# Kernel tuning notes

Hardware: AMD Instinct MI355X
Metric: run time of the kernel (lower is better)

## Reference

```python
import jax, jax.numpy as jnp
import numpy as np

B, S, D_IN, D_H, D_OUT = 32, 1024, 512, 512, 512
N_HEADS, K_NEI = 2, 3
LN_EPS = 1e-5


def _layernorm(x, g, b):
    mu = x.mean(-1, keepdims=True)
    xc = x - mu
    var = (xc * xc).mean(-1, keepdims=True)
    return xc * jax.lax.rsqrt(var + LN_EPS) * g + b


def setup_inputs() -> dict:
    key = jax.random.key(0)
    ks = jax.random.split(key, 8)
    sc = 0.02
    rn = lambda k, shape: jax.random.normal(k, shape, jnp.float32) * sc
    return {
        "x": jax.random.normal(ks[0], (B, S, D_IN), jnp.float32),
        "enc_w": rn(ks[1], (D_H, D_IN)), "enc_b": jnp.zeros((D_H,), jnp.float32),
        "in_w": rn(ks[2], (3 * D_H, D_H)), "in_b": jnp.zeros((3 * D_H,), jnp.float32),
        "out_w": rn(ks[3], (D_H, D_H)), "out_b": jnp.zeros((D_H,), jnp.float32),
        "ln1_g": jnp.ones((D_H,), jnp.float32), "ln1_b": jnp.zeros((D_H,), jnp.float32),
        "ffn_w1": rn(ks[4], (2 * D_H, D_H)), "ffn_b1": jnp.zeros((2 * D_H,), jnp.float32),
        "ffn_w2": rn(ks[5], (D_H, 2 * D_H)), "ffn_b2": jnp.zeros((D_H,), jnp.float32),
        "gc_w": rn(ks[6], (D_H, 2 * D_H)), "gc_b": jnp.zeros((D_H,), jnp.float32),
        "ln2_g": jnp.ones((D_H,), jnp.float32), "ln2_b": jnp.zeros((D_H,), jnp.float32),
        "dec_w": rn(ks[7], (D_OUT, D_H)), "dec_b": jnp.zeros((D_OUT,), jnp.float32),
    }


def reference(x, enc_w, enc_b, in_w, in_b, out_w, out_b, ln1_g, ln1_b,
              ffn_w1, ffn_b1, ffn_w2, ffn_b2, gc_w, gc_b, ln2_g, ln2_b,
              dec_w, dec_b):
    # --- encoder ---
    h = jax.nn.relu(x @ enc_w.T + enc_b)                          # [B,S,Dh]

    # --- ElevateH0toH1: self-attention + LN + residual FFN ---
    qkv = h @ in_w.T + in_b                                       # [B,S,3Dh]
    q, k, v = jnp.split(qkv, 3, axis=-1)
    dh = D_H // N_HEADS
    heads = lambda t: t.reshape(B, S, N_HEADS, dh).transpose(0, 2, 1, 3)
    q, k, v = heads(q), heads(k), heads(v)
    scores = jnp.einsum("bhqd,bhkd->bhqk", q, k) / jnp.sqrt(jnp.float32(dh))
    attn = jax.nn.softmax(scores, axis=-1)
    ctx = jnp.einsum("bhqk,bhkd->bhqd", attn, v)
    ctx = ctx.transpose(0, 2, 1, 3).reshape(B, S, D_H)
    attn_out = ctx @ out_w.T + out_b
    x1 = _layernorm(h + attn_out, ln1_g, ln1_b)
    x1 = x1 + (jax.nn.relu(x1 @ ffn_w1.T + ffn_b1) @ ffn_w2.T + ffn_b2)

    # --- ElevateH1toH2: symmetric KNN adjacency from cosine similarity ---
    nrm = x1 / jnp.maximum(jnp.linalg.norm(x1, axis=-1, keepdims=True), 1e-12)
    sim = jnp.einsum("bid,bjd->bij", nrm, nrm)                    # [B,S,S]
    kk = min(K_NEI, S - 1)
    _, idx = jax.lax.top_k(sim, kk + 1)                           # [B,S,k+1] (incl. self)
    mask = jnp.zeros((B, S, S), bool).at[
        jnp.arange(B)[:, None, None], jnp.arange(S)[None, :, None], idx
    ].set(True)
    mask = mask & ~jnp.eye(S, dtype=bool)                         # drop self edges
    mask = mask | mask.transpose(0, 2, 1)                         # symmetrize
    adj = jnp.where(mask, sim, jnp.float32(0.0))

    nsum = jnp.einsum("bij,bjd->bid", adj, x1)
    cnt = jnp.maximum(adj.sum(-1, keepdims=True), jnp.float32(1.0))
    combined = jnp.concatenate([x1, nsum / cnt], axis=-1)         # [B,S,2Dh]
    out = combined @ gc_w.T + gc_b
    x2 = _layernorm(x1 + out, ln2_g, ln2_b)

    # --- pool + decoder ---
    return x2.mean(axis=1) @ dec_w.T + dec_b                      # [B,D_OUT]
```

## Files before the change

### kernel.cpp

```cpp
#include <hip/hip_runtime.h>
#include <hip/hip_bf16.h>
#include <math.h>

typedef unsigned short u16;
typedef __attribute__((ext_vector_type(8))) short bfrag;
typedef __attribute__((ext_vector_type(4))) float facc;
typedef const __attribute__((address_space(1))) void* gaddr_t;
typedef __attribute__((address_space(3))) void* laddr_t;

#define F_RELU   1
#define F_ROWSC  4
#define F_SIMSC  8
#define F_RESID2 32

__device__ __forceinline__ u16 f2bf(float f) {
  __hip_bfloat16 h = __float2bfloat16(f);
  return *reinterpret_cast<u16*>(&h);
}
__device__ __forceinline__ float bf2f(u16 u) {
  __hip_bfloat16 h = *reinterpret_cast<__hip_bfloat16*>(&u);
  return __bfloat162float(h);
}
__device__ __forceinline__ float wsum(float v) {
#pragma unroll
  for (int o = 32; o; o >>= 1) v += __shfl_xor(v, o);
  return v;
}
__device__ __forceinline__ float wmaxf(float v) {
#pragma unroll
  for (int o = 32; o; o >>= 1) v = fmaxf(v, __shfl_xor(v, o));
  return v;
}

struct GSeg {
  const u16* A; const u16* B;
  long sA, sB;
  int lda, ldb, K;
  int hA, hB;
};

__global__ __launch_bounds__(256)
void bgemm_k(GSeg s0, GSeg s1, GSeg s2, int nseg,
             const float* __restrict__ bias,
             const u16* __restrict__ residH, const u16* __restrict__ residL,
             const float* __restrict__ rsc, const float* __restrict__ csc,
             float* __restrict__ Cf, u16* __restrict__ Cb, u16* __restrict__ Cb2,
             int ldc, long sC, int hC, int headBits, int sS,
             float alpha, int flags, int Mstore)
{
  const int zAll = blockIdx.z;
  const int hIdx = headBits ? (zAll & 1) : 0;
  const int z    = headBits ? (zAll >> 1) : zAll;
  const long cofs = (long)z * sC + (long)hIdx * hC;
  const float* rs = rsc ? rsc + (long)z * sS : nullptr;
  const float* cs = csc ? csc + (long)z * sS : nullptr;

  __shared__ u16 As[128 * 64];
  __shared__ u16 Bs[128 * 64];

  const int tid  = threadIdx.x;
  const int wave = tid >> 6, lane = tid & 63;
  const int m0 = blockIdx.x * 128, n0 = blockIdx.y * 128;
  const int wrow = (wave >> 1) * 64, wcol = (wave & 1) * 64;

  const int lrow = lane >> 3;
  const int lgrp = lane & 7;

  facc acc[4][4];
#pragma unroll
  for (int i = 0; i < 4; ++i)
#pragma unroll
    for (int j = 0; j < 4; ++j) acc[i][j] = (facc)(0.f);

  const int r16 = lane & 15, gq = lane >> 4;

  for (int seg = 0; seg < nseg; ++seg) {
    const GSeg& S = seg == 0 ? s0 : (seg == 1 ? s1 : s2);
    const u16* Ab = S.A + (long)z * S.sA + (long)hIdx * S.hA;
    const u16* Bb = S.B + (long)z * S.sB + (long)hIdx * S.hB;
    for (int k0 = 0; k0 < S.K; k0 += 64) {
#pragma unroll
      for (int ss = 0; ss < 4; ++ss) {
        int rloc = wave * 32 + ss * 8;
        int row  = rloc + lrow;
        int g    = lgrp ^ ((row >> 1) & 7);
        __builtin_amdgcn_global_load_lds(
            (gaddr_t)(const void*)(Ab + (long)(m0 + row) * S.lda + k0 + g * 8),
            (laddr_t)(As + rloc * 64), 16, 0, 0);
        __builtin_amdgcn_global_load_lds(
            (gaddr_t)(const void*)(Bb + (long)(n0 + row) * S.ldb + k0 + g * 8),
            (laddr_t)(Bs + rloc * 64), 16, 0, 0);
      }
      __syncthreads();

#pragma unroll
      for (int kk = 0; kk < 2; ++kk) {
        bfrag af[4], bb[4];
#pragma unroll
        for (int mt = 0; mt < 4; ++mt) {
          int r = wrow + mt * 16 + r16;
          int slot = (kk * 4 + gq) ^ ((r >> 1) & 7);
          af[mt] = *(const bfrag*)&As[r * 64 + slot * 8];
        }
#pragma unroll
        for (int nt = 0; nt < 4; ++nt) {
          int r = wcol + nt * 16 + r16;
          int slot = (kk * 4 + gq) ^ ((r >> 1) & 7);
          bb[nt] = *(const bfrag*)&Bs[r * 64 + slot * 8];
        }
#pragma unroll
        for (int mt = 0; mt < 4; ++mt)
#pragma unroll
          for (int nt = 0; nt < 4; ++nt)
            acc[mt][nt] = __builtin_amdgcn_mfma_f32_16x16x32_bf16(
                af[mt], bb[nt], acc[mt][nt], 0, 0, 0);
      }
      __syncthreads();
    }
  }

#pragma unroll
  for (int mt = 0; mt < 4; ++mt) {
#pragma unroll
    for (int nt = 0; nt < 4; ++nt) {
#pragma unroll
      for (int r = 0; r < 4; ++r) {
        int gm = m0 + wrow + mt * 16 + gq * 4 + r;
        int gn = n0 + wcol + nt * 16 + r16;
        if (gm >= Mstore) continue;
        float v = acc[mt][nt][r] * alpha;
        long ci = cofs + (long)gm * ldc + gn;
        if (flags & F_SIMSC)  v *= rs[gm] * cs[gn];
        if (flags & F_ROWSC)  v *= rs[gm];
        if (bias)             v += bias[gn];
        if (flags & F_RESID2) v += bf2f(residH[ci]) + bf2f(residL[ci]);
        if (flags & F_RELU)   v = fmaxf(v, 0.f);
        if (Cf) Cf[ci] = v;
        if (Cb) {
          u16 hv = f2bf(v);
          Cb[ci] = hv;
          if (Cb2) Cb2[ci] = f2bf(v - bf2f(hv));
        }
      }
    }
  }
}

__global__ __launch_bounds__(256)
void castbf_k(const float* __restrict__ in, u16* __restrict__ out, int n)
{
  int i = blockIdx.x * 256 + threadIdx.x;
  if (i < n) out[i] = f2bf(in[i]);
}

__global__ __launch_bounds__(256)
void castw_k(const float* w0, const float* w1, const float* w2,
             const float* w3, const float* w4, const float* w5,
             const float* w6, u16* __restrict__ dst)
{
  int i = blockIdx.x * 256 + threadIdx.x;
  const float* s; int off;
  if      (i < 262144)  { s = w0; off = 0; }
  else if (i < 1048576) { s = w1; off = 262144; }
  else if (i < 1310720) { s = w2; off = 1048576; }
  else if (i < 1835008) { s = w3; off = 1310720; }
  else if (i < 2359296) { s = w4; off = 1835008; }
  else if (i < 2883584) { s = w5; off = 2359296; }
  else                  { s = w6; off = 2883584; }
  dst[i] = f2bf(s[i - off]);
}

__global__ __launch_bounds__(256)
void ln1_k(const u16* __restrict__ a, const u16* __restrict__ b,
           const float* __restrict__ g, const float* __restrict__ be,
           u16* __restrict__ oh, u16* __restrict__ ol)
{
  long base = (long)blockIdx.x * 512;
  int t = threadIdx.x;
  float v0 = bf2f(a[base + t])       + bf2f(b[base + t]);
  float v1 = bf2f(a[base + t + 256]) + bf2f(b[base + t + 256]);
  __shared__ float red[4], red2[4];
  float s = wsum(v0 + v1);
  if ((t & 63) == 0) red[t >> 6] = s;
  __syncthreads();
  float mean = (red[0] + red[1] + red[2] + red[3]) * (1.f / 512.f);
  float c0 = v0 - mean, c1 = v1 - mean;
  float ss = wsum(c0 * c0 + c1 * c1);
  if ((t & 63) == 0) red2[t >> 6] = ss;
  __syncthreads();
  float var = (red2[0] + red2[1] + red2[2] + red2[3]) * (1.f / 512.f);
  float rstd = rsqrtf(var + 1e-5f);
  float o0 = c0 * rstd * g[t]       + be[t];
  float o1 = c1 * rstd * g[t + 256] + be[t + 256];
  u16 h0 = f2bf(o0), h1 = f2bf(o1);
  oh[base + t] = h0;       oh[base + t + 256] = h1;
  ol[base + t] = f2bf(o0 - bf2f(h0));
  ol[base + t + 256] = f2bf(o1 - bf2f(h1));
}

__global__ __launch_bounds__(256)
void ln2_k(const u16* __restrict__ hi, const u16* __restrict__ lo,
           const u16* __restrict__ b, const float* __restrict__ g,
           const float* __restrict__ be, u16* __restrict__ ob)
{
  long base = (long)blockIdx.x * 512;
  int t = threadIdx.x;
  float v0 = bf2f(hi[base + t])       + bf2f(lo[base + t])       + bf2f(b[base + t]);
  float v1 = bf2f(hi[base + t + 256]) + bf2f(lo[base + t + 256]) + bf2f(b[base + t + 256]);
  __shared__ float red[4], red2[4];
  float s = wsum(v0 + v1);
  if ((t & 63) == 0) red[t >> 6] = s;
  __syncthreads();
  float mean = (red[0] + red[1] + red[2] + red[3]) * (1.f / 512.f);
  float c0 = v0 - mean, c1 = v1 - mean;
  float ss = wsum(c0 * c0 + c1 * c1);
  if ((t & 63) == 0) red2[t >> 6] = ss;
  __syncthreads();
  float var = (red2[0] + red2[1] + red2[2] + red2[3]) * (1.f / 512.f);
  float rstd = rsqrtf(var + 1e-5f);
  ob[base + t]       = f2bf(c0 * rstd * g[t]       + be[t]);
  ob[base + t + 256] = f2bf(c1 * rstd * g[t + 256] + be[t + 256]);
}

__global__ __launch_bounds__(256)
void rownorm_k(const u16* __restrict__ hi, const u16* __restrict__ lo,
               float* __restrict__ invn)
{
  long base = (long)blockIdx.x * 512;
  int t = threadIdx.x;
  float v0 = bf2f(hi[base + t])       + bf2f(lo[base + t]);
  float v1 = bf2f(hi[base + t + 256]) + bf2f(lo[base + t + 256]);
  __shared__ float red[4];
  float s = wsum(v0 * v0 + v1 * v1);
  if ((t & 63) == 0) red[t >> 6] = s;
  __syncthreads();
  if (t == 0) {
    float tot = red[0] + red[1] + red[2] + red[3];
    invn[blockIdx.x] = 1.f / fmaxf(sqrtf(tot), 1e-12f);
  }
}

__global__ __launch_bounds__(256)
void softmaxu_k(u16* __restrict__ sc)
{
  long row = blockIdx.x;
  u16* p = sc + row * 1024;
  int t = threadIdx.x;
  float v[4];
#pragma unroll
  for (int i = 0; i < 4; ++i) v[i] = bf2f(p[t + 256 * i]);
  __shared__ float redm[4], redsum[4];
  float m4 = fmaxf(fmaxf(v[0], v[1]), fmaxf(v[2], v[3]));
  float wm = wmaxf(m4);
  if ((t & 63) == 0) redm[t >> 6] = wm;
  __syncthreads();
  float MX = fmaxf(fmaxf(redm[0], redm[1]), fmaxf(redm[2], redm[3]));
  float s = 0.f;
#pragma unroll
  for (int i = 0; i < 4; ++i) { v[i] = __expf(v[i] - MX); s += v[i]; }
  float ws_ = wsum(s);
  if ((t & 63) == 0) redsum[t >> 6] = ws_;
  __syncthreads();
  float inv = 1.f / (redsum[0] + redsum[1] + redsum[2] + redsum[3]);
#pragma unroll
  for (int i = 0; i < 4; ++i) p[t + 256 * i] = f2bf(v[i] * inv);
}

__global__ __launch_bounds__(256)
void transp_k(const u16* __restrict__ in, u16* __restrict__ out,
              int inStride, int outStride, long sIn, long sOut,
              int hIn, int headBits)
{
  const int zAll = blockIdx.z;
  const int h  = headBits ? (zAll & 1) : 0;
  const int zb = headBits ? (zAll >> 1) : zAll;
  const u16* src = in + (long)zb * sIn + (long)h * hIn;
  u16* dst = out + (long)zAll * sOut;
  const int r0 = blockIdx.x * 64, c0 = blockIdx.y * 64;
  __shared__ u16 tile[64][66];
  const int t = threadIdx.x;
#pragma unroll
  for (int p = 0; p < 16; ++p) {
    int idx = p * 256 + t;
    int r = idx >> 6, c = idx & 63;
    tile[r][c] = src[(long)(r0 + r) * inStride + c0 + c];
  }
  __syncthreads();
#pragma unroll
  for (int p = 0; p < 16; ++p) {
    int idx = p * 256 + t;
    int c = idx >> 6, r = idx & 63;
    dst[(long)(c0 + c) * outStride + r0 + r] = tile[r][c];
  }
}

__global__ __launch_bounds__(64)
void topk_k(const float* __restrict__ sim, int* __restrict__ idx4)
{
  long row = blockIdx.x;
  const float* p = sim + row * 1024;
  int t = threadIdx.x;
  int c0 = -1, c1 = -1, c2 = -1, c3 = -1;
#pragma unroll
  for (int pass = 0; pass < 4; ++pass) {
    float best = -INFINITY;
    int bi = 1 << 30;
    for (int j = t; j < 1024; j += 64) {
      if (j == c0 || j == c1 || j == c2 || j == c3) continue;
      float v = p[j];
      if (v > best || (v == best && j < bi)) { best = v; bi = j; }
    }
#pragma unroll
    for (int off = 32; off; off >>= 1) {
      float ov = __shfl_down(best, off);
      int   oi = __shfl_down(bi, off);
      if (ov > best || (ov == best && oi < bi)) { best = ov; bi = oi; }
    }
    bi = __shfl(bi, 0);
    if (pass == 0) c0 = bi; else if (pass == 1) c1 = bi;
    else if (pass == 2) c2 = bi; else c3 = bi;
  }
  if (t == 0) { int* q = idx4 + row * 4; q[0] = c0; q[1] = c1; q[2] = c2; q[3] = c3; }
}

__global__ __launch_bounds__(256)
void adjbf_k(const float* __restrict__ sim, const int* __restrict__ idx4,
             u16* __restrict__ adjb, float* __restrict__ invcnt)
{
  long row = blockIdx.x;
  int b = (int)(row >> 10);
  int i = (int)(row & 1023);
  const float* prow = sim + row * 1024;
  u16* arow_ = adjb + row * 1024;
  const int* my = idx4 + row * 4;
  int m0 = my[0], m1 = my[1], m2 = my[2], m3 = my[3];
  int t = threadIdx.x;
  float lsum = 0.f;
  for (int j = t; j < 1024; j += 256) {
    float v = prow[j];
    bool present = false;
    if (j != i) {
      present = (j == m0) | (j == m1) | (j == m2) | (j == m3);
      if (!present) {
        const int* oj = idx4 + (((long)b << 10) + j) * 4;
        present = (oj[0] == i) | (oj[1] == i) | (oj[2] == i) | (oj[3] == i);
      }
    }
    float a = present ? v : 0.f;
    arow_[j] = f2bf(a);
    lsum += a;
  }
  __shared__ float red[4];
  float s = wsum(lsum);
  if ((t & 63) == 0) red[t >> 6] = s;
  __syncthreads();
  if (t == 0) {
    float tot = red[0] + red[1] + red[2] + red[3];
    invcnt[row] = 1.f / fmaxf(tot, 1.f);
  }
}

__global__ __launch_bounds__(256)
void poolbf_k(const u16* __restrict__ x2, u16* __restrict__ pooled)
{
  int i = blockIdx.x * 256 + threadIdx.x;
  int b = i >> 9, d = i & 511;
  float s = 0.f;
  if (b < 32) {
    const u16* p = x2 + ((long)b << 10) * 512 + d;
    for (int sdx = 0; sdx < 1024; ++sdx) s += bf2f(p[(long)sdx * 512]);
    s *= (1.f / 1024.f);
  }
  pooled[i] = f2bf(s);
}

static inline GSeg mkseg(const u16* A, const u16* B, int K, int lda, int ldb,
                         long sA = 0, long sB = 0, int hA = 0, int hB = 0)
{
  GSeg s; s.A = A; s.B = B; s.K = K; s.lda = lda; s.ldb = ldb;
  s.sA = sA; s.sB = sB; s.hA = hA; s.hB = hB; return s;
}

static inline void bgemm(hipStream_t st, GSeg s0, GSeg s1, GSeg s2, int nseg,
    const float* bias, const u16* residH, const u16* residL,
    const float* rsc, const float* csc, float* Cf, u16* Cb, u16* Cb2,
    int M, int N, int ldc, long sC, int hC, int headBits, int sS,
    float alpha, int flags, int nz, int Mstore = -1)
{
  dim3 g(M / 128, N / 128, nz);
  bgemm_k<<<g, 256, 0, st>>>(s0, s1, s2, nseg, bias, residH, residL,
                             rsc, csc, Cf, Cb, Cb2, ldc, sC, hC, headBits,
                             sS, alpha, flags, Mstore < 0 ? M : Mstore);
}

extern "C" void kernel_launch(void* const* d_in, const int* in_sizes, int n_in,
                              void* d_out, int out_size, void* d_ws, size_t ws_size,
                              hipStream_t stream)
{
  (void)in_sizes; (void)n_in; (void)out_size;
  const float* x     = (const float*)d_in[0];
  const float* enc_w = (const float*)d_in[1];
  const float* enc_b = (const float*)d_in[2];
  const float* in_w  = (const float*)d_in[3];
  const float* in_b  = (const float*)d_in[4];
  const float* out_w = (const float*)d_in[5];
  const float* out_b = (const float*)d_in[6];
  const float* ln1_g = (const float*)d_in[7];
  const float* ln1_b = (const float*)d_in[8];
  const float* fw1   = (const float*)d_in[9];
  const float* fb1   = (const float*)d_in[10];
  const float* fw2   = (const float*)d_in[11];
  const float* fb2   = (const float*)d_in[12];
  const float* gc_w  = (const float*)d_in[13];
  const float* gc_b  = (const float*)d_in[14];
  const float* ln2_g = (const float*)d_in[15];
  const float* ln2_b = (const float*)d_in[16];
  const float* dec_w = (const float*)d_in[17];
  const float* dec_b = (const float*)d_in[18];
  float* out = (float*)d_out;

  char* base = (char*)d_ws;
  u16*  bf1  = (u16*)(base);
  u16*  lob  = (u16*)(base + 33554432);
  u16*  bf2  = (u16*)(base + 67108864);
  u16*  wgt  = (u16*)(base + 100663296);
  float* invn    = (float*)(base + 106954752);
  float* invcnt  = (float*)(base + 107085824);
  u16*   pooledb = (u16*)(base + 107216896);
  int*   idx4    = (int*)(base + 107347968);
  char*  scr     = base + 107872256;
  const size_t need = 107872256 + 83886080;
  if (ws_size < need) return;

  u16* encw = wgt;
  u16* inw  = wgt + 262144;
  u16* outw = wgt + 1048576;
  u16* fw1b = wgt + 1310720;
  u16* fw2b = wgt + 1835008;
  u16* gcwb = wgt + 2359296;
  u16* decw = wgt + 2883584;

  const int Mtok = 32768;
  GSeg Z = mkseg(nullptr, nullptr, 0, 0, 0);

  u16* xbf = (u16*)scr;
  castbf_k<<<65536, 256, 0, stream>>>(x, xbf, 16777216);
  castw_k<<<12288, 256, 0, stream>>>(enc_w, in_w, out_w, fw1, fw2, gc_w, dec_w, wgt);

  bgemm(stream, mkseg(xbf, encw, 512, 512, 512), Z, Z, 1,
        enc_b, nullptr, nullptr, nullptr, nullptr, nullptr, bf1, nullptr,
        Mtok, 512, 512, 0, 0, 0, 0, 1.f, F_RELU, 1);

  for (int c = 0; c < 4; ++c) {
    long row0 = (long)c * 8192;
    u16* qkvc = (u16*)scr;
    u16* sco  = (u16*)(scr + 25165824);
    u16* vT   = (u16*)(scr + 58720256);
    bgemm(stream, mkseg(bf1 + row0 * 512, inw, 512, 512, 512), Z, Z, 1,
          in_b, nullptr, nullptr, nullptr, nullptr, nullptr, qkvc, nullptr,
          8192, 1536, 1536, 0, 0, 0, 0, 1.f, 0, 1);
    bgemm(stream, mkseg(qkvc, qkvc + 512, 256, 1536, 1536,
                        1572864, 1572864, 256, 256), Z, Z, 1,
          nullptr, nullptr, nullptr, nullptr, nullptr, nullptr, sco, nullptr,
          1024, 1024, 1024, 2097152, 1048576, 1, 0, 0.0625f, 0, 16);
    softmaxu_k<<<16384, 256, 0, stream>>>(sco);
    transp_k<<<dim3(16, 4, 16), 256, 0, stream>>>(
        qkvc + 1024, vT, 1536, 1024, 1572864, 262144, 256, 1);
    bgemm(stream, mkseg(sco, vT, 1024, 1024, 1024,
                        2097152, 524288, 1048576, 262144), Z, Z, 1,
          nullptr, nullptr, nullptr, nullptr, nullptr, nullptr,
          bf2 + row0 * 512, nullptr,
          1024, 256, 512, 524288, 256, 1, 0, 1.f, 0, 16);
  }

  u16* aoc = (u16*)scr;
  bgemm(stream, mkseg(bf2, outw, 512, 512, 512), Z, Z, 1,
        out_b, nullptr, nullptr, nullptr, nullptr, nullptr, aoc, nullptr,
        Mtok, 512, 512, 0, 0, 0, 0, 1.f, 0, 1);

  ln1_k<<<Mtok, 256, 0, stream>>>(bf1, aoc, ln1_g, ln1_b, bf1, lob);

  u16* mid = (u16*)scr;
  bgemm(stream, mkseg(bf1, fw1b, 512, 512, 512), Z, Z, 1,
        fb1, nullptr, nullptr, nullptr, nullptr, nullptr, mid, nullptr,
        Mtok, 1024, 1024, 0, 0, 0, 0, 1.f, F_RELU, 1);
  bgemm(stream, mkseg(mid, fw2b, 1024, 1024, 1024), Z, Z, 1,
        fb2, bf1, lob, nullptr, nullptr, nullptr, bf1, lob,
        Mtok, 512, 512, 0, 0, 0, 0, 1.f, F_RESID2, 1);

  rownorm_k<<<Mtok, 256, 0, stream>>>(bf1, lob, invn);

  float* simc = (float*)scr;
  u16*   adjb = (u16*)(scr + 33554432);
  u16*   x1T  = (u16*)(scr + 50331648);
  transp_k<<<dim3(16, 8, 32), 256, 0, stream>>>(bf1, x1T, 512, 1024,
                                                524288, 524288, 0, 0);
  for (int g = 0; g < 4; ++g) {
    long row0 = (long)g * 8192;
    bgemm(stream,
          mkseg(bf1 + row0 * 512, bf1 + row0 * 512, 512, 512, 512, 524288, 524288),
          mkseg(bf1 + row0 * 512, lob + row0 * 512, 512, 512, 512, 524288, 524288),
          mkseg(lob + row0 * 512, bf1 + row0 * 512, 512, 512, 512, 524288, 524288),
          3, nullptr, nullptr, nullptr, invn + row0, invn + row0,
          simc, nullptr, nullptr,
          1024, 1024, 1024, 1048576, 0, 0, 1024, 1.f, F_SIMSC, 8);
    topk_k<<<8192, 64, 0, stream>>>(simc, idx4 + row0 * 4);
    adjbf_k<<<8192, 256, 0, stream>>>(simc, idx4 + row0 * 4, adjb, invcnt + row0);
    bgemm(stream, mkseg(adjb, x1T + row0 * 512, 1024, 1024, 1024,
                        1048576, 524288), Z, Z, 1,
          nullptr, nullptr, nullptr, invcnt + row0, nullptr, nullptr,
          bf2 + row0 * 512, nullptr,
          1024, 512, 512, 524288, 0, 0, 1024, 1.f, F_ROWSC, 8);
  }

  u16* gch = (u16*)scr;
  bgemm(stream, mkseg(bf1, gcwb, 512, 512, 1024),
        mkseg(bf2, gcwb + 512, 512, 512, 1024), Z, 2,
        gc_b, nullptr, nullptr, nullptr, nullptr, nullptr, gch, nullptr,
        Mtok, 512, 512, 0, 0, 0, 0, 1.f, 0, 1);

  ln2_k<<<Mtok, 256, 0, stream>>>(bf1, lob, gch, ln2_g, ln2_b, bf2);

  poolbf_k<<<256, 256, 0, stream>>>(bf2, pooledb);
  bgemm(stream, mkseg(pooledb, decw, 512, 512, 512), Z, Z, 1,
        dec_b, nullptr, nullptr, nullptr, nullptr, out, nullptr, nullptr,
        128, 512, 512, 0, 0, 0, 0, 1.f, 0, 1, 32);
}
```

Measured before the change: 1.612 ms.

## Double-buffer GEMM LDS tiles and drop hi/lo correction in similarity GEMM

The batched GEMM kernel now uses two LDS buffers per operand and issues the global-to-LDS loads for the next K tile before computing on the current one. This removes one barrier per iteration and overlaps memory with MFMA work. The segment loop is flattened into a single iteration count across up to three segments. The cosine-similarity GEMM also drops the two low-order correction segments and uses only the bf16 high part, cutting its work to a third. This risks changing which top-k neighbours are selected.

```diff
diff --git a/kernel.cpp b/kernel.cpp
--- a/kernel.cpp
+++ b/kernel.cpp
@@ -40,7 +40,7 @@
 };
 
 __global__ __launch_bounds__(256)
-void bgemm_k(GSeg s0, GSeg s1, GSeg s2, int nseg,
+void bgemm_k(GSeg s0, GSeg s1, GSeg s2,
              const float* __restrict__ bias,
              const u16* __restrict__ residH, const u16* __restrict__ residL,
              const float* __restrict__ rsc, const float* __restrict__ csc,
@@ -55,14 +55,27 @@
   const float* rs = rsc ? rsc + (long)z * sS : nullptr;
   const float* cs = csc ? csc + (long)z * sS : nullptr;
 
-  __shared__ u16 As[128 * 64];
-  __shared__ u16 Bs[128 * 64];
+  __shared__ u16 As[2][128 * 64];
+  __shared__ u16 Bs[2][128 * 64];
 
   const int tid  = threadIdx.x;
   const int wave = tid >> 6, lane = tid & 63;
   const int m0 = blockIdx.x * 128, n0 = blockIdx.y * 128;
   const int wrow = (wave >> 1) * 64, wcol = (wave & 1) * 64;
 
+  const u16* ApS[3]; const u16* BpS[3]; int ldaS[3], ldbS[3];
+  ApS[0] = s0.A + (long)z * s0.sA + (long)hIdx * s0.hA;
+  BpS[0] = s0.B + (long)z * s0.sB + (long)hIdx * s0.hB;
+  ldaS[0] = s0.lda; ldbS[0] = s0.ldb;
+  ApS[1] = s1.A ? s1.A + (long)z * s1.sA + (long)hIdx * s1.hA : nullptr;
+  BpS[1] = s1.B ? s1.B + (long)z * s1.sB + (long)hIdx * s1.hB : nullptr;
+  ldaS[1] = s1.lda; ldbS[1] = s1.ldb;
+  ApS[2] = s2.A ? s2.A + (long)z * s2.sA + (long)hIdx * s2.hA : nullptr;
+  BpS[2] = s2.B ? s2.B + (long)z * s2.sB + (long)hIdx * s2.hB : nullptr;
+  ldaS[2] = s2.lda; ldbS[2] = s2.ldb;
+  const int n0i = s0.K >> 6, n1i = n0i + (s1.K >> 6);
+  const int nIt = n1i + (s2.K >> 6);
+
   const int lrow = lane >> 3;
   const int lgrp = lane & 7;
 
@@ -74,48 +87,56 @@
 
   const int r16 = lane & 15, gq = lane >> 4;
 
-  for (int seg = 0; seg < nseg; ++seg) {
-    const GSeg& S = seg == 0 ? s0 : (seg == 1 ? s1 : s2);
-    const u16* Ab = S.A + (long)z * S.sA + (long)hIdx * S.hA;
-    const u16* Bb = S.B + (long)z * S.sB + (long)hIdx * S.hB;
-    for (int k0 = 0; k0 < S.K; k0 += 64) {
-#pragma unroll
-      for (int ss = 0; ss < 4; ++ss) {
-        int rloc = wave * 32 + ss * 8;
-        int row  = rloc + lrow;
-        int g    = lgrp ^ ((row >> 1) & 7);
-        __builtin_amdgcn_global_load_lds(
-            (gaddr_t)(const void*)(Ab + (long)(m0 + row) * S.lda + k0 + g * 8),
-            (laddr_t)(As + rloc * 64), 16, 0, 0);
-        __builtin_amdgcn_global_load_lds(
-            (gaddr_t)(const void*)(Bb + (long)(n0 + row) * S.ldb + k0 + g * 8),
-            (laddr_t)(Bs + rloc * 64), 16, 0, 0);
+  auto stage = [&](int buf, int it) {
+    int sidx, base;
+    if (it < n0i)      { sidx = 0; base = 0; }
+    else if (it < n1i) { sidx = 1; base = n0i; }
+    else               { sidx = 2; base = n1i; }
+    const int k0 = (it - base) << 6;
+    const u16* Ab = ApS[sidx];
+    const u16* Bb = BpS[sidx];
+    const int la = ldaS[sidx], lb = ldbS[sidx];
+#pragma unroll
+    for (int ss = 0; ss < 4; ++ss) {
+      int rloc = wave * 32 + ss * 8;
+      int row  = rloc + lrow;
+      int g    = lgrp ^ ((row >> 1) & 7);
+      __builtin_amdgcn_global_load_lds(
+          (gaddr_t)(const void*)(Ab + (long)(m0 + row) * la + k0 + g * 8),
+          (laddr_t)(As[buf] + rloc * 64), 16, 0, 0);
+      __builtin_amdgcn_global_load_lds(
+          (gaddr_t)(const void*)(Bb + (long)(n0 + row) * lb + k0 + g * 8),
+          (laddr_t)(Bs[buf] + rloc * 64), 16, 0, 0);
+    }
+  };
+
+  stage(0, 0);
+  for (int it = 0; it < nIt; ++it) {
+    const int buf = it & 1;
+    __syncthreads();
+    if (it + 1 < nIt) stage(buf ^ 1, it + 1);
+
+#pragma unroll
+    for (int kk = 0; kk < 2; ++kk) {
+      bfrag af[4], bb[4];
+#pragma unroll
+      for (int mt = 0; mt < 4; ++mt) {
+        int r = wrow + mt * 16 + r16;
+        int slot = (kk * 4 + gq) ^ ((r >> 1) & 7);
+        af[mt] = *(const bfrag*)&As[buf][r * 64 + slot * 8];
       }
-      __syncthreads();
-
-#pragma unroll
-      for (int kk = 0; kk < 2; ++kk) {
-        bfrag af[4], bb[4];
-#pragma unroll
-        for (int mt = 0; mt < 4; ++mt) {
-          int r = wrow + mt * 16 + r16;
-          int slot = (kk * 4 + gq) ^ ((r >> 1) & 7);
-          af[mt] = *(const bfrag*)&As[r * 64 + slot * 8];
-        }
-#pragma unroll
-        for (int nt = 0; nt < 4; ++nt) {
-          int r = wcol + nt * 16 + r16;
-          int slot = (kk * 4 + gq) ^ ((r >> 1) & 7);
-          bb[nt] = *(const bfrag*)&Bs[r * 64 + slot * 8];
-        }
-#pragma unroll
-        for (int mt = 0; mt < 4; ++mt)
-#pragma unroll
-          for (int nt = 0; nt < 4; ++nt)
-            acc[mt][nt] = __builtin_amdgcn_mfma_f32_16x16x32_bf16(
-                af[mt], bb[nt], acc[mt][nt], 0, 0, 0);
+#pragma unroll
+      for (int nt = 0; nt < 4; ++nt) {
+        int r = wcol + nt * 16 + r16;
+        int slot = (kk * 4 + gq) ^ ((r >> 1) & 7);
+        bb[nt] = *(const bfrag*)&Bs[buf][r * 64 + slot * 8];
       }
-      __syncthreads();
+#pragma unroll
+      for (int mt = 0; mt < 4; ++mt)
+#pragma unroll
+        for (int nt = 0; nt < 4; ++nt)
+          acc[mt][nt] = __builtin_amdgcn_mfma_f32_16x16x32_bf16(
+              af[mt], bb[nt], acc[mt][nt], 0, 0, 0);
     }
   }
 
@@ -381,14 +402,14 @@
   s.sA = sA; s.sB = sB; s.hA = hA; s.hB = hB; return s;
 }
 
-static inline void bgemm(hipStream_t st, GSeg s0, GSeg s1, GSeg s2, int nseg,
+static inline void bgemm(hipStream_t st, GSeg s0, GSeg s1, GSeg s2,
     const float* bias, const u16* residH, const u16* residL,
     const float* rsc, const float* csc, float* Cf, u16* Cb, u16* Cb2,
     int M, int N, int ldc, long sC, int hC, int headBits, int sS,
     float alpha, int flags, int nz, int Mstore = -1)
 {
   dim3 g(M / 128, N / 128, nz);
-  bgemm_k<<<g, 256, 0, st>>>(s0, s1, s2, nseg, bias, residH, residL,
+  bgemm_k<<<g, 256, 0, st>>>(s0, s1, s2, bias, residH, residL,
                              rsc, csc, Cf, Cb, Cb2, ldc, sC, hC, headBits,
                              sS, alpha, flags, Mstore < 0 ? M : Mstore);
 }
@@ -447,7 +468,7 @@
   castbf_k<<<65536, 256, 0, stream>>>(x, xbf, 16777216);
   castw_k<<<12288, 256, 0, stream>>>(enc_w, in_w, out_w, fw1, fw2, gc_w, dec_w, wgt);
 
-  bgemm(stream, mkseg(xbf, encw, 512, 512, 512), Z, Z, 1,
+  bgemm(stream, mkseg(xbf, encw, 512, 512, 512), Z, Z,
         enc_b, nullptr, nullptr, nullptr, nullptr, nullptr, bf1, nullptr,
         Mtok, 512, 512, 0, 0, 0, 0, 1.f, F_RELU, 1);
 
@@ -456,35 +477,35 @@
     u16* qkvc = (u16*)scr;
     u16* sco  = (u16*)(scr + 25165824);
     u16* vT   = (u16*)(scr + 58720256);
-    bgemm(stream, mkseg(bf1 + row0 * 512, inw, 512, 512, 512), Z, Z, 1,
+    bgemm(stream, mkseg(bf1 + row0 * 512, inw, 512, 512, 512), Z, Z,
           in_b, nullptr, nullptr, nullptr, nullptr, nullptr, qkvc, nullptr,
           8192, 1536, 1536, 0, 0, 0, 0, 1.f, 0, 1);
     bgemm(stream, mkseg(qkvc, qkvc + 512, 256, 1536, 1536,
-                        1572864, 1572864, 256, 256), Z, Z, 1,
+                        1572864, 1572864, 256, 256), Z, Z,
           nullptr, nullptr, nullptr, nullptr, nullptr, nullptr, sco, nullptr,
           1024, 1024, 1024, 2097152, 1048576, 1, 0, 0.0625f, 0, 16);
     softmaxu_k<<<16384, 256, 0, stream>>>(sco);
     transp_k<<<dim3(16, 4, 16), 256, 0, stream>>>(
         qkvc + 1024, vT, 1536, 1024, 1572864, 262144, 256, 1);
     bgemm(stream, mkseg(sco, vT, 1024, 1024, 1024,
-                        2097152, 524288, 1048576, 262144), Z, Z, 1,
+                        2097152, 524288, 1048576, 262144), Z, Z,
           nullptr, nullptr, nullptr, nullptr, nullptr, nullptr,
           bf2 + row0 * 512, nullptr,
           1024, 256, 512, 524288, 256, 1, 0, 1.f, 0, 16);
   }
 
   u16* aoc = (u16*)scr;
-  bgemm(stream, mkseg(bf2, outw, 512, 512, 512), Z, Z, 1,
+  bgemm(stream, mkseg(bf2, outw, 512, 512, 512), Z, Z,
         out_b, nullptr, nullptr, nullptr, nullptr, nullptr, aoc, nullptr,
         Mtok, 512, 512, 0, 0, 0, 0, 1.f, 0, 1);
 
   ln1_k<<<Mtok, 256, 0, stream>>>(bf1, aoc, ln1_g, ln1_b, bf1, lob);
 
   u16* mid = (u16*)scr;
-  bgemm(stream, mkseg(bf1, fw1b, 512, 512, 512), Z, Z, 1,
+  bgemm(stream, mkseg(bf1, fw1b, 512, 512, 512), Z, Z,
         fb1, nullptr, nullptr, nullptr, nullptr, nullptr, mid, nullptr,
         Mtok, 1024, 1024, 0, 0, 0, 0, 1.f, F_RELU, 1);
-  bgemm(stream, mkseg(mid, fw2b, 1024, 1024, 1024), Z, Z, 1,
+  bgemm(stream, mkseg(mid, fw2b, 1024, 1024, 1024), Z, Z,
         fb2, bf1, lob, nullptr, nullptr, nullptr, bf1, lob,
         Mtok, 512, 512, 0, 0, 0, 0, 1.f, F_RESID2, 1);
 
@@ -499,15 +520,13 @@
     long row0 = (long)g * 8192;
     bgemm(stream,
           mkseg(bf1 + row0 * 512, bf1 + row0 * 512, 512, 512, 512, 524288, 524288),
-          mkseg(bf1 + row0 * 512, lob + row0 * 512, 512, 512, 512, 524288, 524288),
-          mkseg(lob + row0 * 512, bf1 + row0 * 512, 512, 512, 512, 524288, 524288),
-          3, nullptr, nullptr, nullptr, invn + row0, invn + row0,
+          Z, Z, nullptr, nullptr, nullptr, invn + row0, invn + row0,
           simc, nullptr, nullptr,
           1024, 1024, 1024, 1048576, 0, 0, 1024, 1.f, F_SIMSC, 8);
     topk_k<<<8192, 64, 0, stream>>>(simc, idx4 + row0 * 4);
     adjbf_k<<<8192, 256, 0, stream>>>(simc, idx4 + row0 * 4, adjb, invcnt + row0);
     bgemm(stream, mkseg(adjb, x1T + row0 * 512, 1024, 1024, 1024,
-                        1048576, 524288), Z, Z, 1,
+                        1048576, 524288), Z, Z,
           nullptr, nullptr, nullptr, invcnt + row0, nullptr, nullptr,
           bf2 + row0 * 512, nullptr,
           1024, 512, 512, 524288, 0, 0, 1024, 1.f, F_ROWSC, 8);
@@ -515,14 +534,14 @@
 
   u16* gch = (u16*)scr;
   bgemm(stream, mkseg(bf1, gcwb, 512, 512, 1024),
-        mkseg(bf2, gcwb + 512, 512, 512, 1024), Z, 2,
+        mkseg(bf2, gcwb + 512, 512, 512, 1024), Z,
         gc_b, nullptr, nullptr, nullptr, nullptr, nullptr, gch, nullptr,
         Mtok, 512, 512, 0, 0, 0, 0, 1.f, 0, 1);
 
   ln2_k<<<Mtok, 256, 0, stream>>>(bf1, lob, gch, ln2_g, ln2_b, bf2);
 
   poolbf_k<<<256, 256, 0, stream>>>(bf2, pooledb);
-  bgemm(stream, mkseg(pooledb, decw, 512, 512, 512), Z, Z, 1,
+  bgemm(stream, mkseg(pooledb, decw, 512, 512, 512), Z, Z,
         dec_b, nullptr, nullptr, nullptr, nullptr, out, nullptr, nullptr,
         128, 512, 512, 0, 0, 0, 0, 1.f, 0, 1, 32);
 }
```

Measured after the change: 1.605 ms. No clear change (-0.4%).
